# Performance work log

Hardware: AMD Instinct MI355X
Metric: run time of the kernel (lower is better)

Reference implementation:

```python
import jax, jax.numpy as jnp
import numpy as np

TOP_K = 2
LN_EPS = 1e-5
GATE_EPS = 1e-6


def setup_inputs() -> dict:
    key = jax.random.key(0)
    ks = jax.random.split(key, 5)
    B, D, E, H, O = 16384, 1200, 8, 1024, 1
    x = jax.random.normal(ks[0], (B, D), dtype=jnp.float32)
    w_gate = jax.random.normal(ks[1], (D, E), dtype=jnp.float32) * 0.05
    W1 = jax.random.normal(ks[2], (E, D, H), dtype=jnp.float32) * (1.0 / np.sqrt(D))
    b1 = jnp.zeros((E, H), dtype=jnp.float32)
    g1 = jnp.ones((E, H), dtype=jnp.float32)   # LayerNorm weight
    be1 = jnp.zeros((E, H), dtype=jnp.float32)  # LayerNorm bias
    W2 = jax.random.normal(ks[3], (E, H, O), dtype=jnp.float32) * (1.0 / np.sqrt(H))
    b2 = jnp.zeros((E, O), dtype=jnp.float32)
    return {"x": x, "w_gate": w_gate, "W1": W1, "b1": b1, "g1": g1, "be1": be1, "W2": W2, "b2": b2}


def reference(x, w_gate, W1, b1, g1, be1, W2, b2):
    B = x.shape[0]
    # --- top-k gating (eval mode: no noise) ---
    probs = jax.nn.softmax(x @ w_gate, axis=1)                 # [B, E]
    top_vals, top_idx = jax.lax.top_k(probs, TOP_K)            # [B, k]
    top_gates = top_vals / (jnp.sum(top_vals, axis=1, keepdims=True) + GATE_EPS)
    gates = jnp.zeros_like(probs).at[jnp.arange(B)[:, None], top_idx].set(top_gates)  # [B, E]
    # --- per-expert MLP (computed densely for all experts; gates zero out non-selected) ---
    h = jnp.einsum('bd,edh->beh', x, W1) + b1                  # [B, E, H]
    mu = jnp.mean(h, axis=-1, keepdims=True)
    var = jnp.var(h, axis=-1, keepdims=True)
    h = (h - mu) * jax.lax.rsqrt(var + LN_EPS) * g1 + be1      # LayerNorm
    h = jax.nn.relu(h)
    out = jax.nn.sigmoid(jnp.einsum('beh,eho->beo', h, W2) + b2)  # [B, E, O]
    # --- scatter/combine: weighted sum over experts ---
    y = jnp.einsum('be,beo->bo', gates, out)                   # [B, O]
    return y
```

## Files before the change

kernel.cpp:

```cpp
#include <hip/hip_runtime.h>
#include <hip/hip_bf16.h>
#include <stdint.h>

#define B_ROWS 16384
#define D_IN   1200
#define D_PAD  1216
#define N_EXP  8
#define H_DIM  1024
#define R_CAP  4608
#define CAP    36864
#define N_RT   288
#define LN_EPS 1e-5f
#define GATE_EPS 1e-6f
#define CNT_STRIDE 16

#define O_CNT    0
#define O_PROWC  512
#define O_PGATEC 147968
#define O_XBF    295424
#define O_W1T    40143744
#define O_HBUF   60066688

#define GATING_BLOCKS (B_ROWS / 16)
#define W1T_BLOCKS    (19 * 16 * 8)

typedef short bf16x8 __attribute__((ext_vector_type(8)));
typedef short short8 __attribute__((ext_vector_type(8)));
typedef short short4v __attribute__((ext_vector_type(4)));
typedef float f32x4 __attribute__((ext_vector_type(4)));

__device__ __forceinline__ void load_lds16(const void* gptr, void* ldsptr) {
    __builtin_amdgcn_global_load_lds(
        (__attribute__((address_space(1))) void*)const_cast<void*>(gptr),
        (__attribute__((address_space(3))) void*)ldsptr, 16, 0, 0);
}

__device__ __forceinline__ short4v pack_bf16x4(float4 a) {
    union { short4v v; __hip_bfloat16 h[4]; } u;
    u.h[0] = __float2bfloat16(a.x); u.h[1] = __float2bfloat16(a.y);
    u.h[2] = __float2bfloat16(a.z); u.h[3] = __float2bfloat16(a.w);
    return u.v;
}

__global__ __launch_bounds__(256) void gating_kernel(
    const float* __restrict__ x, const float* __restrict__ wg,
    int* __restrict__ cnt, int* __restrict__ pairRowC, float* __restrict__ pairGateC,
    __hip_bfloat16* __restrict__ xbf, float* __restrict__ y)
{
    __shared__ int lcnt[N_EXP];
    __shared__ int base[N_EXP];
    int bx = blockIdx.x;
    int tid = threadIdx.x;

    if (bx == GATING_BLOCKS) {
        short8* xrow = (short8*)(xbf + (long)B_ROWS * D_PAD);
        if (tid < 152) xrow[tid] = (short8){0, 0, 0, 0, 0, 0, 0, 0};
        return;
    }

    if (tid < N_EXP) lcnt[tid] = 0;
    if (tid < 16) y[bx * 16 + tid] = 0.f;
    __syncthreads();

    int widx = tid >> 6;
    int lane = tid & 63;
    int rowbase = bx * 16 + widx * 4;
    const float* xw = x + (long)rowbase * D_IN;

    float acc[4][8];
#pragma unroll
    for (int r = 0; r < 4; ++r)
#pragma unroll
        for (int e = 0; e < N_EXP; ++e) acc[r][e] = 0.f;

    for (int i = lane; i < 304; i += 64) {
        if (i < 300) {
            const float4* wv4 = (const float4*)(wg + (long)i * 32);
            float4 w0 = wv4[0], w1v = wv4[1], w2 = wv4[2], w3 = wv4[3],
                   w4 = wv4[4], w5 = wv4[5], w6 = wv4[6], w7 = wv4[7];
#pragma unroll
            for (int r = 0; r < 4; ++r) {
                float4 xv = ((const float4*)(xw + (long)r * D_IN))[i];
                acc[r][0] += xv.x * w0.x + xv.y * w2.x + xv.z * w4.x + xv.w * w6.x;
                acc[r][1] += xv.x * w0.y + xv.y * w2.y + xv.z * w4.y + xv.w * w6.y;
                acc[r][2] += xv.x * w0.z + xv.y * w2.z + xv.z * w4.z + xv.w * w6.z;
                acc[r][3] += xv.x * w0.w + xv.y * w2.w + xv.z * w4.w + xv.w * w6.w;
                acc[r][4] += xv.x * w1v.x + xv.y * w3.x + xv.z * w5.x + xv.w * w7.x;
                acc[r][5] += xv.x * w1v.y + xv.y * w3.y + xv.z * w5.y + xv.w * w7.y;
                acc[r][6] += xv.x * w1v.z + xv.y * w3.z + xv.z * w5.z + xv.w * w7.z;
                acc[r][7] += xv.x * w1v.w + xv.y * w3.w + xv.z * w5.w + xv.w * w7.w;
                ((short4v*)(xbf + (long)(rowbase + r) * D_PAD))[i] = pack_bf16x4(xv);
            }
        } else {
#pragma unroll
            for (int r = 0; r < 4; ++r)
                ((short4v*)(xbf + (long)(rowbase + r) * D_PAD))[i] = (short4v){0, 0, 0, 0};
        }
    }

#pragma unroll
    for (int r = 0; r < 4; ++r)
#pragma unroll
        for (int e = 0; e < N_EXP; ++e) {
            float v = acc[r][e];
#pragma unroll
            for (int off = 32; off > 0; off >>= 1) v += __shfl_xor(v, off, 64);
            acc[r][e] = v;
        }

    float my[N_EXP];
#pragma unroll
    for (int e = 0; e < N_EXP; ++e) my[e] = acc[0][e];
#pragma unroll
    for (int r = 1; r < 4; ++r)
#pragma unroll
        for (int e = 0; e < N_EXP; ++e)
            if (lane == r) my[e] = acc[r][e];

    int i0 = 0, i1 = 1, s0 = 0, s1 = 0;
    float g0 = 0.f, g1 = 0.f;
    if (lane < 4) {
        float m = my[0];
#pragma unroll
        for (int e = 1; e < N_EXP; ++e) m = fmaxf(m, my[e]);
        float p[N_EXP], s = 0.f;
#pragma unroll
        for (int e = 0; e < N_EXP; ++e) { p[e] = expf(my[e] - m); s += p[e]; }
#pragma unroll
        for (int e = 1; e < N_EXP; ++e) if (p[e] > p[i0]) i0 = e;
        i1 = (i0 == 0) ? 1 : 0;
#pragma unroll
        for (int e = 0; e < N_EXP; ++e) if (e != i0 && p[e] > p[i1]) i1 = e;
        float v0 = p[i0] / s, v1 = p[i1] / s;
        float inv = 1.f / (v0 + v1 + GATE_EPS);
        g0 = v0 * inv; g1 = v1 * inv;
        s0 = atomicAdd(&lcnt[i0], 1);
        s1 = atomicAdd(&lcnt[i1], 1);
    }
    __syncthreads();
    if (tid < N_EXP) base[tid] = atomicAdd(&cnt[tid * CNT_STRIDE], lcnt[tid]);
    __syncthreads();
    if (lane < 4) {
        int row = rowbase + lane;
        int p0 = i0 * R_CAP + base[i0] + s0;
        pairRowC[p0] = row; pairGateC[p0] = g0;
        int p1 = i1 * R_CAP + base[i1] + s1;
        pairRowC[p1] = row; pairGateC[p1] = g1;
    }
}

__global__ __launch_bounds__(256) void w1t_kernel(
    const float* __restrict__ W1, __hip_bfloat16* __restrict__ w1t)
{
    __shared__ float tile[2][32][33];
    int b = blockIdx.x;
    int tid = threadIdx.x;
    int d0 = (b % 19) * 64;
    int h0 = ((b / 19) % 16) * 64;
    int e = b / (19 * 16);
    const float* src = W1 + (long)e * D_IN * H_DIM;

    int hs = tid & 15;
    int dr = tid >> 4;
#pragma unroll
    for (int s = 0; s < 4; ++s) {
        int dl = dr + 16 * s;
        int d = d0 + dl;
        float4 v = (d < D_IN)
            ? ((const float4*)(src + (long)d * H_DIM + h0))[hs]
            : (float4){0.f, 0.f, 0.f, 0.f};
        int drl = dl & 31;
        int hl = hs * 4;
        int Th = hl >> 5;
        int hh = hl & 31;
        tile[Th][drl][hh + 0] = v.x;
        tile[Th][drl][hh + 1] = v.y;
        tile[Th][drl][hh + 2] = v.z;
        tile[Th][drl][hh + 3] = v.w;
        if (s == 1) {
            __syncthreads();
            int T2 = tid >> 7, rr = tid & 127;
            int hl2 = rr >> 2, dseg = rr & 3;
            float f[8];
#pragma unroll
            for (int j = 0; j < 8; ++j) f[j] = tile[T2][dseg * 8 + j][hl2];
            union { short8 v8; __hip_bfloat16 hh8[8]; } u;
#pragma unroll
            for (int j = 0; j < 8; ++j) u.hh8[j] = __float2bfloat16(f[j]);
            int h = h0 + T2 * 32 + hl2;
            ((short8*)(w1t + (long)e * H_DIM * D_PAD + (long)h * D_PAD + d0))[dseg] = u.v8;
            __syncthreads();
        }
    }
    __syncthreads();
    {
        int T2 = tid >> 7, rr = tid & 127;
        int hl2 = rr >> 2, dseg = rr & 3;
        float f[8];
#pragma unroll
        for (int j = 0; j < 8; ++j) f[j] = tile[T2][dseg * 8 + j][hl2];
        union { short8 v8; __hip_bfloat16 hh8[8]; } u;
#pragma unroll
        for (int j = 0; j < 8; ++j) u.hh8[j] = __float2bfloat16(f[j]);
        int h = h0 + T2 * 32 + hl2;
        ((short8*)(w1t + (long)e * H_DIM * D_PAD + (long)h * D_PAD + d0 + 32))[dseg] = u.v8;
    }
}

__global__ __launch_bounds__(256) void gemm_kernel(
    const __hip_bfloat16* __restrict__ xbf, const __hip_bfloat16* __restrict__ w1t,
    const float* __restrict__ b1, const int* __restrict__ cnt,
    const int* __restrict__ pairRowC,
    __hip_bfloat16* __restrict__ hbuf)
{
    int bi = blockIdx.x;
    int xcd = bi & 7;
    int j = bi >> 3;
    int col0 = (j & 7) << 7;
    int rt = xcd * 36 + (j >> 3);
    int row0 = rt << 7;
    int e = xcd;
    int cnt_e = cnt[e * CNT_STRIDE];
    if (row0 - e * R_CAP >= cnt_e) return;

    __shared__ short lA[128 * 32];
    __shared__ short lB[128 * 32];

    int t = threadIdx.x;
    int lane = t & 63, w = t >> 6;
    int wm = (w >> 1) * 64, wn = (w & 1) * 64;
    int l15 = lane & 15, quad = lane >> 4;
    int qsw = quad ^ ((l15 >> 1) & 3);

    f32x4 acc[4][4];
#pragma unroll
    for (int i = 0; i < 4; ++i)
#pragma unroll
        for (int j2 = 0; j2 < 4; ++j2) acc[i][j2] = (f32x4){0.f, 0.f, 0.f, 0.f};

    int r1 = t >> 2, seg = t & 3;
    int sw = seg ^ ((r1 >> 1) & 3);
    int ridx1 = pairRowC[row0 + r1];
    int ridx2 = pairRowC[row0 + 64 + r1];
    ridx1 = ((unsigned)ridx1 > B_ROWS) ? B_ROWS : ridx1;
    ridx2 = ((unsigned)ridx2 > B_ROWS) ? B_ROWS : ridx2;
    const __hip_bfloat16* Arow1 = xbf + (long)ridx1 * D_PAD + sw * 8;
    const __hip_bfloat16* Arow2 = xbf + (long)ridx2 * D_PAD + sw * 8;
    const __hip_bfloat16* Bb = w1t + (long)e * H_DIM * D_PAD + (long)col0 * D_PAD;
    const __hip_bfloat16* Brow1 = Bb + (long)r1 * D_PAD + sw * 8;
    const __hip_bfloat16* Brow2 = Bb + (long)(r1 + 64) * D_PAD + sw * 8;
    char* lAc = (char*)lA;
    char* lBc = (char*)lB;

    for (int kt = 0; kt < D_PAD / 32; ++kt) {
        __syncthreads();
        int k0 = kt * 32;
        load_lds16(Arow1 + k0, lAc + t * 16);
        load_lds16(Arow2 + k0, lAc + t * 16 + 4096);
        load_lds16(Brow1 + k0, lBc + t * 16);
        load_lds16(Brow2 + k0, lBc + t * 16 + 4096);
        __syncthreads();

        bf16x8 af[4], bfr[4];
#pragma unroll
        for (int i = 0; i < 4; ++i)
            af[i] = *(const bf16x8*)(lAc + (wm + i * 16 + l15) * 64 + qsw * 16);
#pragma unroll
        for (int j2 = 0; j2 < 4; ++j2)
            bfr[j2] = *(const bf16x8*)(lBc + (wn + j2 * 16 + l15) * 64 + qsw * 16);
#pragma unroll
        for (int i = 0; i < 4; ++i)
#pragma unroll
            for (int j2 = 0; j2 < 4; ++j2)
                acc[i][j2] = __builtin_amdgcn_mfma_f32_16x16x32_bf16(af[i], bfr[j2], acc[i][j2], 0, 0, 0);
    }

#pragma unroll
    for (int i = 0; i < 4; ++i) {
        int lr = wm + i * 16 + quad * 4;
#pragma unroll
        for (int j2 = 0; j2 < 4; ++j2) {
            int gc = col0 + wn + j2 * 16 + l15;
            float bias = b1[e * H_DIM + gc];
#pragma unroll
            for (int r = 0; r < 4; ++r) {
                float v = acc[i][j2][r] + bias;
                hbuf[(long)(row0 + lr + r) * H_DIM + gc] = __float2bfloat16(v);
            }
        }
    }
}

__global__ __launch_bounds__(256) void ln_head_kernel(
    const __hip_bfloat16* __restrict__ hbuf, const int* __restrict__ cnt,
    const int* __restrict__ pairRowC, const float* __restrict__ pairGateC,
    const float* __restrict__ g1, const float* __restrict__ be1,
    const float* __restrict__ W2, const float* __restrict__ b2,
    float* __restrict__ y)
{
    int tid = threadIdx.x;
    int p = blockIdx.x * 4 + (tid >> 6);
    int e = p / R_CAP;
    int slot = p - e * R_CAP;
    if (slot >= cnt[e * CNT_STRIDE]) return;

    int lane = tid & 63;
    int row = pairRowC[p];
    float gate = pairGateC[p];
    const short4v* hr = (const short4v*)(hbuf + (long)p * H_DIM);

    float v[16];
    float sum = 0.f, sumsq = 0.f;
#pragma unroll
    for (int k = 0; k < 4; ++k) {
        union { short4v s; __hip_bfloat16 h[4]; } hv;
        hv.s = hr[lane + k * 64];
#pragma unroll
        for (int j = 0; j < 4; ++j) {
            float f = __bfloat162float(hv.h[j]);
            v[k * 4 + j] = f;
            sum += f;
            sumsq += f * f;
        }
    }
#pragma unroll
    for (int off = 32; off > 0; off >>= 1) {
        sum += __shfl_xor(sum, off, 64);
        sumsq += __shfl_xor(sumsq, off, 64);
    }
    float mu = sum * (1.f / H_DIM);
    float var = sumsq * (1.f / H_DIM) - mu * mu;
    float rstd = rsqrtf(var + LN_EPS);

    float z = 0.f;
#pragma unroll
    for (int k = 0; k < 4; ++k) {
        float4 gv = ((const float4*)(g1 + e * H_DIM))[lane + k * 64];
        float4 bv = ((const float4*)(be1 + e * H_DIM))[lane + k * 64];
        float4 wv = ((const float4*)(W2 + e * H_DIM))[lane + k * 64];
        z += fmaxf((v[k*4+0] - mu) * rstd * gv.x + bv.x, 0.f) * wv.x;
        z += fmaxf((v[k*4+1] - mu) * rstd * gv.y + bv.y, 0.f) * wv.y;
        z += fmaxf((v[k*4+2] - mu) * rstd * gv.z + bv.z, 0.f) * wv.z;
        z += fmaxf((v[k*4+3] - mu) * rstd * gv.w + bv.w, 0.f) * wv.w;
    }
#pragma unroll
    for (int off = 32; off > 0; off >>= 1) z += __shfl_xor(z, off, 64);
    if (lane == 0) {
        float zt = z + b2[e];
        float o = 1.f / (1.f + expf(-zt));
        atomicAdd(&y[row], gate * o);
    }
}

extern "C" void kernel_launch(void* const* d_in, const int* in_sizes, int n_in,
                              void* d_out, int out_size, void* d_ws, size_t ws_size,
                              hipStream_t stream)
{
    const float* x   = (const float*)d_in[0];
    const float* wg  = (const float*)d_in[1];
    const float* W1  = (const float*)d_in[2];
    const float* b1  = (const float*)d_in[3];
    const float* g1  = (const float*)d_in[4];
    const float* be1 = (const float*)d_in[5];
    const float* W2  = (const float*)d_in[6];
    const float* b2  = (const float*)d_in[7];
    float* y = (float*)d_out;

    char* ws = (char*)d_ws;
    int*   cnt       = (int*)(ws + O_CNT);
    int*   pairRowC  = (int*)(ws + O_PROWC);
    float* pairGateC = (float*)(ws + O_PGATEC);
    __hip_bfloat16* xbf  = (__hip_bfloat16*)(ws + O_XBF);
    __hip_bfloat16* w1t  = (__hip_bfloat16*)(ws + O_W1T);
    __hip_bfloat16* hbuf = (__hip_bfloat16*)(ws + O_HBUF);

    hipMemsetAsync(cnt, 0, 512, stream);

    gating_kernel<<<GATING_BLOCKS + 1, 256, 0, stream>>>(x, wg, cnt, pairRowC,
                                                         pairGateC, xbf, y);
    w1t_kernel<<<W1T_BLOCKS, 256, 0, stream>>>(W1, w1t);
    gemm_kernel<<<N_RT * 8, 256, 0, stream>>>(xbf, w1t, b1, cnt, pairRowC, hbuf);
    ln_head_kernel<<<CAP / 4, 256, 0, stream>>>(hbuf, cnt, pairRowC, pairGateC,
                                                g1, be1, W2, b2, y);
}
```

Baseline: 304.5 us.

## Enlarge grouped GEMM tiles to 256x256 with 4-stage async LDS pipeline

Rewrites the expert GEMM to use 512-thread blocks computing 256x256 output tiles, with a four-buffer LDS ring fed by direct global-to-LDS loads issued three k-steps ahead. MFMA work is split into two halves, interleaved with staging of A and B, and uses explicit waitcnt, barriers and setprio. The goal is more reuse per loaded byte and hiding global load latency behind matrix math, in place of the old single-buffered 128x128 loop that synchronized twice per step. The cost is 128KB of LDS per block and 128 accumulator registers per thread, which limits occupancy to one block per CU, and coarser tiles waste more work on partially filled expert row tiles.

```diff
diff --git a/kernel.cpp b/kernel.cpp
--- a/kernel.cpp
+++ b/kernel.cpp
@@ -9,7 +9,6 @@
 #define H_DIM  1024
 #define R_CAP  4608
 #define CAP    36864
-#define N_RT   288
 #define LN_EPS 1e-5f
 #define GATE_EPS 1e-6f
 #define CNT_STRIDE 16
@@ -23,6 +22,10 @@
 
 #define GATING_BLOCKS (B_ROWS / 16)
 #define W1T_BLOCKS    (19 * 16 * 8)
+
+#define NT        (D_PAD / 32)
+#define LDS_BUF   32768
+#define GEMM_BLOCKS (N_EXP * (R_CAP / 256) * (H_DIM / 256))
 
 typedef short bf16x8 __attribute__((ext_vector_type(8)));
 typedef short short8 __attribute__((ext_vector_type(8)));
@@ -207,76 +210,117 @@
     }
 }
 
-__global__ __launch_bounds__(256) void gemm_kernel(
+__global__ __launch_bounds__(512) void gemm_kernel(
     const __hip_bfloat16* __restrict__ xbf, const __hip_bfloat16* __restrict__ w1t,
     const float* __restrict__ b1, const int* __restrict__ cnt,
     const int* __restrict__ pairRowC,
     __hip_bfloat16* __restrict__ hbuf)
 {
+    __shared__ __attribute__((aligned(128))) char lds[4 * LDS_BUF];
+
     int bi = blockIdx.x;
-    int xcd = bi & 7;
+    int e = bi & 7;
     int j = bi >> 3;
-    int col0 = (j & 7) << 7;
-    int rt = xcd * 36 + (j >> 3);
-    int row0 = rt << 7;
-    int e = xcd;
+    int ct = j & 3;
+    int rt = j >> 2;
     int cnt_e = cnt[e * CNT_STRIDE];
-    if (row0 - e * R_CAP >= cnt_e) return;
-
-    __shared__ short lA[128 * 32];
-    __shared__ short lB[128 * 32];
+    if (rt * 256 >= cnt_e) return;
+    int row0 = e * R_CAP + rt * 256;
+    int col0 = ct * 256;
 
     int t = threadIdx.x;
     int lane = t & 63, w = t >> 6;
-    int wm = (w >> 1) * 64, wn = (w & 1) * 64;
+    int wm = (w >> 2) << 7;
+    int wn = (w & 3) << 6;
     int l15 = lane & 15, quad = lane >> 4;
     int qsw = quad ^ ((l15 >> 1) & 3);
-
-    f32x4 acc[4][4];
-#pragma unroll
-    for (int i = 0; i < 4; ++i)
-#pragma unroll
-        for (int j2 = 0; j2 < 4; ++j2) acc[i][j2] = (f32x4){0.f, 0.f, 0.f, 0.f};
 
     int r1 = t >> 2, seg = t & 3;
     int sw = seg ^ ((r1 >> 1) & 3);
     int ridx1 = pairRowC[row0 + r1];
-    int ridx2 = pairRowC[row0 + 64 + r1];
+    int ridx2 = pairRowC[row0 + 128 + r1];
     ridx1 = ((unsigned)ridx1 > B_ROWS) ? B_ROWS : ridx1;
     ridx2 = ((unsigned)ridx2 > B_ROWS) ? B_ROWS : ridx2;
     const __hip_bfloat16* Arow1 = xbf + (long)ridx1 * D_PAD + sw * 8;
     const __hip_bfloat16* Arow2 = xbf + (long)ridx2 * D_PAD + sw * 8;
     const __hip_bfloat16* Bb = w1t + (long)e * H_DIM * D_PAD + (long)col0 * D_PAD;
     const __hip_bfloat16* Brow1 = Bb + (long)r1 * D_PAD + sw * 8;
-    const __hip_bfloat16* Brow2 = Bb + (long)(r1 + 64) * D_PAD + sw * 8;
-    char* lAc = (char*)lA;
-    char* lBc = (char*)lB;
-
-    for (int kt = 0; kt < D_PAD / 32; ++kt) {
-        __syncthreads();
-        int k0 = kt * 32;
-        load_lds16(Arow1 + k0, lAc + t * 16);
-        load_lds16(Arow2 + k0, lAc + t * 16 + 4096);
-        load_lds16(Brow1 + k0, lBc + t * 16);
-        load_lds16(Brow2 + k0, lBc + t * 16 + 4096);
-        __syncthreads();
-
-        bf16x8 af[4], bfr[4];
-#pragma unroll
-        for (int i = 0; i < 4; ++i)
-            af[i] = *(const bf16x8*)(lAc + (wm + i * 16 + l15) * 64 + qsw * 16);
-#pragma unroll
-        for (int j2 = 0; j2 < 4; ++j2)
-            bfr[j2] = *(const bf16x8*)(lBc + (wn + j2 * 16 + l15) * 64 + qsw * 16);
-#pragma unroll
-        for (int i = 0; i < 4; ++i)
-#pragma unroll
-            for (int j2 = 0; j2 < 4; ++j2)
+    const __hip_bfloat16* Brow2 = Bb + (long)(r1 + 128) * D_PAD + sw * 8;
+
+#define STAGE_A(wbuf, koff) do { \
+    load_lds16(Arow1 + (koff), lds + (wbuf) * LDS_BUF + t * 16); \
+    load_lds16(Arow2 + (koff), lds + (wbuf) * LDS_BUF + 8192 + t * 16); } while (0)
+#define STAGE_B(wbuf, koff) do { \
+    load_lds16(Brow1 + (koff), lds + (wbuf) * LDS_BUF + 16384 + t * 16); \
+    load_lds16(Brow2 + (koff), lds + (wbuf) * LDS_BUF + 24576 + t * 16); } while (0)
+
+    f32x4 acc[8][4];
+#pragma unroll
+    for (int i = 0; i < 8; ++i)
+#pragma unroll
+        for (int j2 = 0; j2 < 4; ++j2) acc[i][j2] = (f32x4){0.f, 0.f, 0.f, 0.f};
+
+    STAGE_A(0, 0);  STAGE_B(0, 0);
+    STAGE_A(1, 32); STAGE_B(1, 32);
+    STAGE_A(2, 64); STAGE_B(2, 64);
+    asm volatile("s_waitcnt vmcnt(8)" ::: "memory");
+    __builtin_amdgcn_s_barrier();
+
+    int rb = 0;
+#pragma unroll 1
+    for (int kt = 0; kt < NT; ++kt) {
+        char* ldsA = lds + rb * LDS_BUF;
+        char* ldsB = ldsA + 16384;
+        int wb = rb + 3; if (wb >= 4) wb -= 4;
+        bool doStage = (kt + 3 < NT);
+        int koff = (kt + 3) * 32;
+
+        bf16x8 af[8], bfr[4];
+#pragma unroll
+        for (int i = 0; i < 8; ++i)
+            af[i] = *(const bf16x8*)(ldsA + (wm + i * 16 + l15) * 64 + qsw * 16);
+#pragma unroll
+        for (int j2 = 0; j2 < 2; ++j2)
+            bfr[j2] = *(const bf16x8*)(ldsB + (wn + j2 * 16 + l15) * 64 + qsw * 16);
+        if (doStage) STAGE_A(wb, koff);
+        __builtin_amdgcn_s_barrier();
+        asm volatile("s_waitcnt lgkmcnt(0)" ::: "memory");
+        __builtin_amdgcn_sched_barrier(0);
+        __builtin_amdgcn_s_setprio(1);
+#pragma unroll
+        for (int i = 0; i < 8; ++i)
+#pragma unroll
+            for (int j2 = 0; j2 < 2; ++j2)
                 acc[i][j2] = __builtin_amdgcn_mfma_f32_16x16x32_bf16(af[i], bfr[j2], acc[i][j2], 0, 0, 0);
-    }
-
-#pragma unroll
-    for (int i = 0; i < 4; ++i) {
+        __builtin_amdgcn_s_setprio(0);
+        __builtin_amdgcn_s_barrier();
+
+#pragma unroll
+        for (int j2 = 2; j2 < 4; ++j2)
+            bfr[j2] = *(const bf16x8*)(ldsB + (wn + j2 * 16 + l15) * 64 + qsw * 16);
+        if (doStage) STAGE_B(wb, koff);
+        __builtin_amdgcn_s_barrier();
+        asm volatile("s_waitcnt lgkmcnt(0)" ::: "memory");
+        __builtin_amdgcn_sched_barrier(0);
+        __builtin_amdgcn_s_setprio(1);
+#pragma unroll
+        for (int i = 0; i < 8; ++i)
+#pragma unroll
+            for (int j2 = 2; j2 < 4; ++j2)
+                acc[i][j2] = __builtin_amdgcn_mfma_f32_16x16x32_bf16(af[i], bfr[j2], acc[i][j2], 0, 0, 0);
+        __builtin_amdgcn_s_setprio(0);
+        if (kt < NT - 3)       asm volatile("s_waitcnt vmcnt(8)" ::: "memory");
+        else if (kt == NT - 3) asm volatile("s_waitcnt vmcnt(4)" ::: "memory");
+        else                   asm volatile("s_waitcnt vmcnt(0)" ::: "memory");
+        __builtin_amdgcn_s_barrier();
+
+        rb += 1; if (rb >= 4) rb -= 4;
+    }
+#undef STAGE_A
+#undef STAGE_B
+
+#pragma unroll
+    for (int i = 0; i < 8; ++i) {
         int lr = wm + i * 16 + quad * 4;
 #pragma unroll
         for (int j2 = 0; j2 < 4; ++j2) {
@@ -379,7 +423,7 @@
     gating_kernel<<<GATING_BLOCKS + 1, 256, 0, stream>>>(x, wg, cnt, pairRowC,
                                                          pairGateC, xbf, y);
     w1t_kernel<<<W1T_BLOCKS, 256, 0, stream>>>(W1, w1t);
-    gemm_kernel<<<N_RT * 8, 256, 0, stream>>>(xbf, w1t, b1, cnt, pairRowC, hbuf);
+    gemm_kernel<<<GEMM_BLOCKS, 512, 0, stream>>>(xbf, w1t, b1, cnt, pairRowC, hbuf);
     ln_head_kernel<<<CAP / 4, 256, 0, stream>>>(hbuf, cnt, pairRowC, pairGateC,
                                                 g1, be1, W2, b2, y);
 }
```

After: 325.9 us. +7.0%, slower.

## Triple-buffer GEMM LDS loads and merge gating with W1 transpose kernel

Applied to the files above, without the earlier changes.

The GEMM main loop now uses a three-slot LDS ring, issuing global-to-LDS loads two K-tiles ahead. It waits with vmcnt counts and one barrier per iteration instead of two full barriers, so memory latency overlaps the MFMA work. Separately, the gating and W1 transpose/convert kernels are fused into one launch by block-index dispatch, which removes a launch and lets both run concurrently. The costs are more LDS per block (48KB), which may lower occupancy, and a fused kernel whose LDS footprint is the union of both branches.

```diff
diff --git a/kernel.cpp b/kernel.cpp
--- a/kernel.cpp
+++ b/kernel.cpp
@@ -23,6 +23,10 @@
 
 #define GATING_BLOCKS (B_ROWS / 16)
 #define W1T_BLOCKS    (19 * 16 * 8)
+#define PREP_BLOCKS   (GATING_BLOCKS + 1 + W1T_BLOCKS)
+
+#define NT        (D_PAD / 32)
+#define SLOT_SZ   16384
 
 typedef short bf16x8 __attribute__((ext_vector_type(8)));
 typedef short short8 __attribute__((ext_vector_type(8)));
@@ -42,15 +46,72 @@
     return u.v;
 }
 
-__global__ __launch_bounds__(256) void gating_kernel(
+__global__ __launch_bounds__(256) void prep_kernel(
     const float* __restrict__ x, const float* __restrict__ wg,
     int* __restrict__ cnt, int* __restrict__ pairRowC, float* __restrict__ pairGateC,
-    __hip_bfloat16* __restrict__ xbf, float* __restrict__ y)
+    __hip_bfloat16* __restrict__ xbf, float* __restrict__ y,
+    const float* __restrict__ W1, __hip_bfloat16* __restrict__ w1t)
 {
     __shared__ int lcnt[N_EXP];
     __shared__ int base[N_EXP];
+    __shared__ float tile[2][32][33];
     int bx = blockIdx.x;
     int tid = threadIdx.x;
+
+    if (bx > GATING_BLOCKS) {
+        int b = bx - GATING_BLOCKS - 1;
+        int d0 = (b % 19) * 64;
+        int h0 = ((b / 19) % 16) * 64;
+        int e = b / (19 * 16);
+        const float* src = W1 + (long)e * D_IN * H_DIM;
+
+        int hs = tid & 15;
+        int dr = tid >> 4;
+#pragma unroll
+        for (int s = 0; s < 4; ++s) {
+            int dl = dr + 16 * s;
+            int d = d0 + dl;
+            float4 v = (d < D_IN)
+                ? ((const float4*)(src + (long)d * H_DIM + h0))[hs]
+                : (float4){0.f, 0.f, 0.f, 0.f};
+            int drl = dl & 31;
+            int hl = hs * 4;
+            int Th = hl >> 5;
+            int hh = hl & 31;
+            tile[Th][drl][hh + 0] = v.x;
+            tile[Th][drl][hh + 1] = v.y;
+            tile[Th][drl][hh + 2] = v.z;
+            tile[Th][drl][hh + 3] = v.w;
+            if (s == 1) {
+                __syncthreads();
+                int T2 = tid >> 7, rr = tid & 127;
+                int hl2 = rr >> 2, dseg = rr & 3;
+                float f[8];
+#pragma unroll
+                for (int jj = 0; jj < 8; ++jj) f[jj] = tile[T2][dseg * 8 + jj][hl2];
+                union { short8 v8; __hip_bfloat16 hh8[8]; } u;
+#pragma unroll
+                for (int jj = 0; jj < 8; ++jj) u.hh8[jj] = __float2bfloat16(f[jj]);
+                int h = h0 + T2 * 32 + hl2;
+                ((short8*)(w1t + (long)e * H_DIM * D_PAD + (long)h * D_PAD + d0))[dseg] = u.v8;
+                __syncthreads();
+            }
+        }
+        __syncthreads();
+        {
+            int T2 = tid >> 7, rr = tid & 127;
+            int hl2 = rr >> 2, dseg = rr & 3;
+            float f[8];
+#pragma unroll
+            for (int jj = 0; jj < 8; ++jj) f[jj] = tile[T2][dseg * 8 + jj][hl2];
+            union { short8 v8; __hip_bfloat16 hh8[8]; } u;
+#pragma unroll
+            for (int jj = 0; jj < 8; ++jj) u.hh8[jj] = __float2bfloat16(f[jj]);
+            int h = h0 + T2 * 32 + hl2;
+            ((short8*)(w1t + (long)e * H_DIM * D_PAD + (long)h * D_PAD + d0 + 32))[dseg] = u.v8;
+        }
+        return;
+    }
 
     if (bx == GATING_BLOCKS) {
         short8* xrow = (short8*)(xbf + (long)B_ROWS * D_PAD);
@@ -146,64 +207,6 @@
         pairRowC[p0] = row; pairGateC[p0] = g0;
         int p1 = i1 * R_CAP + base[i1] + s1;
         pairRowC[p1] = row; pairGateC[p1] = g1;
-    }
-}
-
-__global__ __launch_bounds__(256) void w1t_kernel(
-    const float* __restrict__ W1, __hip_bfloat16* __restrict__ w1t)
-{
-    __shared__ float tile[2][32][33];
-    int b = blockIdx.x;
-    int tid = threadIdx.x;
-    int d0 = (b % 19) * 64;
-    int h0 = ((b / 19) % 16) * 64;
-    int e = b / (19 * 16);
-    const float* src = W1 + (long)e * D_IN * H_DIM;
-
-    int hs = tid & 15;
-    int dr = tid >> 4;
-#pragma unroll
-    for (int s = 0; s < 4; ++s) {
-        int dl = dr + 16 * s;
-        int d = d0 + dl;
-        float4 v = (d < D_IN)
-            ? ((const float4*)(src + (long)d * H_DIM + h0))[hs]
-            : (float4){0.f, 0.f, 0.f, 0.f};
-        int drl = dl & 31;
-        int hl = hs * 4;
-        int Th = hl >> 5;
-        int hh = hl & 31;
-        tile[Th][drl][hh + 0] = v.x;
-        tile[Th][drl][hh + 1] = v.y;
-        tile[Th][drl][hh + 2] = v.z;
-        tile[Th][drl][hh + 3] = v.w;
-        if (s == 1) {
-            __syncthreads();
-            int T2 = tid >> 7, rr = tid & 127;
-            int hl2 = rr >> 2, dseg = rr & 3;
-            float f[8];
-#pragma unroll
-            for (int j = 0; j < 8; ++j) f[j] = tile[T2][dseg * 8 + j][hl2];
-            union { short8 v8; __hip_bfloat16 hh8[8]; } u;
-#pragma unroll
-            for (int j = 0; j < 8; ++j) u.hh8[j] = __float2bfloat16(f[j]);
-            int h = h0 + T2 * 32 + hl2;
-            ((short8*)(w1t + (long)e * H_DIM * D_PAD + (long)h * D_PAD + d0))[dseg] = u.v8;
-            __syncthreads();
-        }
-    }
-    __syncthreads();
-    {
-        int T2 = tid >> 7, rr = tid & 127;
-        int hl2 = rr >> 2, dseg = rr & 3;
-        float f[8];
-#pragma unroll
-        for (int j = 0; j < 8; ++j) f[j] = tile[T2][dseg * 8 + j][hl2];
-        union { short8 v8; __hip_bfloat16 hh8[8]; } u;
-#pragma unroll
-        for (int j = 0; j < 8; ++j) u.hh8[j] = __float2bfloat16(f[j]);
-        int h = h0 + T2 * 32 + hl2;
-        ((short8*)(w1t + (long)e * H_DIM * D_PAD + (long)h * D_PAD + d0 + 32))[dseg] = u.v8;
     }
 }
 
@@ -223,8 +226,7 @@
     int cnt_e = cnt[e * CNT_STRIDE];
     if (row0 - e * R_CAP >= cnt_e) return;
 
-    __shared__ short lA[128 * 32];
-    __shared__ short lB[128 * 32];
+    __shared__ __attribute__((aligned(128))) char lds[3 * SLOT_SZ];
 
     int t = threadIdx.x;
     int lane = t & 63, w = t >> 6;
@@ -249,18 +251,27 @@
     const __hip_bfloat16* Bb = w1t + (long)e * H_DIM * D_PAD + (long)col0 * D_PAD;
     const __hip_bfloat16* Brow1 = Bb + (long)r1 * D_PAD + sw * 8;
     const __hip_bfloat16* Brow2 = Bb + (long)(r1 + 64) * D_PAD + sw * 8;
-    char* lAc = (char*)lA;
-    char* lBc = (char*)lB;
-
-    for (int kt = 0; kt < D_PAD / 32; ++kt) {
-        __syncthreads();
-        int k0 = kt * 32;
-        load_lds16(Arow1 + k0, lAc + t * 16);
-        load_lds16(Arow2 + k0, lAc + t * 16 + 4096);
-        load_lds16(Brow1 + k0, lBc + t * 16);
-        load_lds16(Brow2 + k0, lBc + t * 16 + 4096);
-        __syncthreads();
-
+
+#define STAGE(sl, koff) do { \
+    char* sb_ = lds + (sl) * SLOT_SZ; \
+    load_lds16(Arow1 + (koff), sb_ + t * 16); \
+    load_lds16(Arow2 + (koff), sb_ + 4096 + t * 16); \
+    load_lds16(Brow1 + (koff), sb_ + 8192 + t * 16); \
+    load_lds16(Brow2 + (koff), sb_ + 12288 + t * 16); } while (0)
+
+    STAGE(0, 0);
+    STAGE(1, 32);
+    asm volatile("s_waitcnt vmcnt(4)" ::: "memory");
+    __builtin_amdgcn_s_barrier();
+    asm volatile("" ::: "memory");
+
+    int cur = 0;
+    for (int kt = 0; kt < NT; ++kt) {
+        int nxt2 = cur + 2; if (nxt2 >= 3) nxt2 -= 3;
+        if (kt + 2 < NT) STAGE(nxt2, (kt + 2) * 32);
+
+        const char* lAc = lds + cur * SLOT_SZ;
+        const char* lBc = lAc + 8192;
         bf16x8 af[4], bfr[4];
 #pragma unroll
         for (int i = 0; i < 4; ++i)
@@ -273,7 +284,16 @@
 #pragma unroll
             for (int j2 = 0; j2 < 4; ++j2)
                 acc[i][j2] = __builtin_amdgcn_mfma_f32_16x16x32_bf16(af[i], bfr[j2], acc[i][j2], 0, 0, 0);
-    }
+
+        if (kt + 2 < NT)      asm volatile("s_waitcnt vmcnt(4)" ::: "memory");
+        else if (kt + 1 < NT) asm volatile("s_waitcnt vmcnt(0)" ::: "memory");
+        if (kt + 1 < NT) {
+            __builtin_amdgcn_s_barrier();
+            asm volatile("" ::: "memory");
+        }
+        cur += 1; if (cur >= 3) cur -= 3;
+    }
+#undef STAGE
 
 #pragma unroll
     for (int i = 0; i < 4; ++i) {
@@ -376,9 +396,8 @@
 
     hipMemsetAsync(cnt, 0, 512, stream);
 
-    gating_kernel<<<GATING_BLOCKS + 1, 256, 0, stream>>>(x, wg, cnt, pairRowC,
-                                                         pairGateC, xbf, y);
-    w1t_kernel<<<W1T_BLOCKS, 256, 0, stream>>>(W1, w1t);
+    prep_kernel<<<PREP_BLOCKS, 256, 0, stream>>>(x, wg, cnt, pairRowC, pairGateC,
+                                                 xbf, y, W1, w1t);
     gemm_kernel<<<N_RT * 8, 256, 0, stream>>>(xbf, w1t, b1, cnt, pairRowC, hbuf);
     ln_head_kernel<<<CAP / 4, 256, 0, stream>>>(hbuf, cnt, pairRowC, pairGateC,
                                                 g1, be1, W2, b2, y);
```

After: 307.4 us. Within noise of the previous version (+0.9%).
